# Kernel optimization log

Hardware: AMD Instinct MI355X
Metric: run time of the kernel (lower is better)

Reference implementation:

```python
import jax, jax.numpy as jnp
import numpy as np
import math

B, S, E, H = 4, 2048, 1024, 16

def setup_inputs() -> dict:
    key = jax.random.key(0)
    k1, k2, k3 = jax.random.split(key, 3)
    scale_in = 1.0 / math.sqrt(E)
    x = jax.random.normal(k1, (B, S, E), dtype=jnp.float32)
    W_attn = jax.random.normal(k2, (E, 3 * E), dtype=jnp.float32) * scale_in
    b_attn = jnp.zeros((3 * E,), dtype=jnp.float32)
    W_proj = jax.random.normal(k3, (E, E), dtype=jnp.float32) * scale_in
    b_proj = jnp.zeros((E,), dtype=jnp.float32)
    return {"x": x, "W_attn": W_attn, "b_attn": b_attn, "W_proj": W_proj, "b_proj": b_proj}

def reference(x, W_attn, b_attn, W_proj, b_proj):
    batch, seq, emb = x.shape
    hd = emb // H  # head_dim
    qkv = x @ W_attn + b_attn                      # [B,S,3E]
    q, k, v = jnp.split(qkv, 3, axis=-1)
    # [B,S,E] -> [B,H,S,hd]
    q = q.reshape(batch, seq, H, hd).transpose(0, 2, 1, 3)
    k = k.reshape(batch, seq, H, hd).transpose(0, 2, 1, 3)
    v = v.reshape(batch, seq, H, hd).transpose(0, 2, 1, 3)
    scores = jnp.einsum('bhqd,bhkd->bhqk', q, k) * (1.0 / math.sqrt(hd))
    causal = jnp.tril(jnp.ones((seq, seq), dtype=bool))
    scores = jnp.where(causal[None, None, :, :], scores, jnp.finfo(scores.dtype).min)
    attn = jax.nn.softmax(scores, axis=-1)         # dropout p=0 -> identity
    out = jnp.einsum('bhqk,bhkd->bhqd', attn, v)   # [B,H,S,hd]
    out = out.transpose(0, 2, 1, 3).reshape(batch, seq, emb)
    return out @ W_proj + b_proj
```

## Files before the change

kernel.cpp:

```cpp
#include <hip/hip_runtime.h>

typedef __bf16 bf16;
typedef __bf16 bf16x8_t __attribute__((ext_vector_type(8)));
typedef __bf16 bf16x4_t __attribute__((ext_vector_type(4)));
typedef __bf16 bf16x2_t __attribute__((ext_vector_type(2)));
typedef float f32x4_t __attribute__((ext_vector_type(4)));

#define S_ 2048
#define E_ 1024
#define HD 64
#define LOG2E 1.4426950408889634f
#define QSCALE (0.125f * LOG2E)

__device__ __forceinline__ void gl_lds16(const bf16* g, bf16* l) {
  __builtin_amdgcn_global_load_lds(
      (const __attribute__((address_space(1))) unsigned int*)g,
      (__attribute__((address_space(3))) unsigned int*)l, 16, 0, 0);
}

__global__ void cvt4(const float* __restrict__ in, bf16* __restrict__ out) {
  int i = (blockIdx.x * 256 + threadIdx.x) * 4;
  float4 v = *(const float4*)(in + i);
  bf16x4_t o = { (bf16)v.x, (bf16)v.y, (bf16)v.z, (bf16)v.w };
  *(bf16x4_t*)(out + i) = o;
}

__global__ void transpose_cvt(const float* __restrict__ in, bf16* __restrict__ out,
                              int R, int C) {
  __shared__ float tile[32][33];
  int c0 = blockIdx.x * 32, r0 = blockIdx.y * 32;
  int tx = threadIdx.x & 31, ty = threadIdx.x >> 5;
#pragma unroll
  for (int i = 0; i < 32; i += 8)
    tile[ty + i][tx] = in[(size_t)(r0 + ty + i) * C + c0 + tx];
  __syncthreads();
#pragma unroll
  for (int i = 0; i < 32; i += 8)
    out[(size_t)(c0 + ty + i) * R + r0 + tx] = (bf16)tile[tx][ty + i];
}

template <int MODE>
__global__ __launch_bounds__(256, 3)
void gemm128(const bf16* __restrict__ A, const bf16* __restrict__ Bt,
             const float* __restrict__ bias,
             bf16* __restrict__ Q, bf16* __restrict__ K, bf16* __restrict__ Vt,
             float* __restrict__ Out) {
  __shared__ __align__(16) bf16 As[128 * 64];
  __shared__ __align__(16) bf16 Bs[128 * 64];
  const int tid = threadIdx.x;
  const int wave = tid >> 6, lane = tid & 63;
  const int quad = lane >> 4, l16 = lane & 15;
  const int wm = wave >> 1, wn = wave & 1;
  const int bm = blockIdx.x, bn = blockIdx.y;

  f32x4_t acc[4][4];
#pragma unroll
  for (int i = 0; i < 4; i++)
#pragma unroll
    for (int j = 0; j < 4; j++) acc[i][j] = (f32x4_t){0.f, 0.f, 0.f, 0.f};

  for (int k0 = 0; k0 < 1024; k0 += 64) {
    __syncthreads();
#pragma unroll
    for (int it = 0; it < 4; it++) {
      int id = it * 256 + tid;
      int row = id >> 3, c = id & 7;
      int sc = (c ^ (row & 7)) * 8;
      gl_lds16(A + (size_t)(bm * 128 + row) * 1024 + k0 + sc, As + id * 8);
      gl_lds16(Bt + (size_t)(bn * 128 + row) * 1024 + k0 + sc, Bs + id * 8);
    }
    __syncthreads();
#pragma unroll
    for (int ks = 0; ks < 2; ks++) {
      bf16x8_t af[4], bfr[4];
#pragma unroll
      for (int i = 0; i < 4; i++) {
        int row = wm * 64 + i * 16 + l16;
        af[i] = *(const bf16x8_t*)&As[row * 64 + (((ks * 4 + quad) ^ (row & 7)) * 8)];
      }
#pragma unroll
      for (int j = 0; j < 4; j++) {
        int row = wn * 64 + j * 16 + l16;
        bfr[j] = *(const bf16x8_t*)&Bs[row * 64 + (((ks * 4 + quad) ^ (row & 7)) * 8)];
      }
#pragma unroll
      for (int i = 0; i < 4; i++)
#pragma unroll
        for (int j = 0; j < 4; j++)
          acc[i][j] = __builtin_amdgcn_mfma_f32_16x16x32_bf16(af[i], bfr[j], acc[i][j], 0, 0, 0);
    }
  }

  if (MODE == 0) {
#pragma unroll
    for (int j = 0; j < 4; j++) {
      int n_g = bn * 128 + wn * 64 + j * 16 + l16;
      float bv = bias[n_g];
      int which = n_g >> 10;
      int cc = n_g & 1023;
      int hh = cc >> 6, dd = cc & 63;
#pragma unroll
      for (int i = 0; i < 4; i++) {
        int m0 = bm * 128 + wm * 64 + i * 16 + quad * 4;
        int bb = m0 >> 11, ss0 = m0 & 2047;
        int bhn = bb * 16 + hh;
        if (which == 2) {
          bf16x4_t pk;
#pragma unroll
          for (int r = 0; r < 4; r++) pk[r] = (bf16)(acc[i][j][r] + bv);
          *(bf16x4_t*)&Vt[((size_t)bhn * 64 + dd) * 2048 + ss0] = pk;
        } else {
          bf16* dst = (which == 0) ? Q : K;
          float scl = (which == 0) ? QSCALE : 1.f;
#pragma unroll
          for (int r = 0; r < 4; r++)
            dst[((size_t)bhn * 2048 + ss0 + r) * 64 + dd] = (bf16)((acc[i][j][r] + bv) * scl);
        }
      }
    }
  } else {
#pragma unroll
    for (int j = 0; j < 4; j++) {
      int n_g = bn * 128 + wn * 64 + j * 16 + l16;
      float bv = bias[n_g];
#pragma unroll
      for (int i = 0; i < 4; i++) {
        int m0 = bm * 128 + wm * 64 + i * 16 + quad * 4;
#pragma unroll
        for (int r = 0; r < 4; r++)
          Out[(size_t)(m0 + r) * 1024 + n_g] = acc[i][j][r] + bv;
      }
    }
  }
}

__global__ __launch_bounds__(256, 3)
void attn_kernel(const bf16* __restrict__ Q, const bf16* __restrict__ K,
                 const bf16* __restrict__ Vt, bf16* __restrict__ O) {
  __shared__ __align__(16) bf16 Ks[128 * 64];
  __shared__ __align__(16) bf16 Vs[64 * 128];
  __shared__ __align__(16) int Ps[4][32 * 36];
  const int tid = threadIdx.x;
  const int wave = tid >> 6, lane = tid & 63;
  const int quad = lane >> 4, l16 = lane & 15;
  const int qb = 15 - blockIdx.x, bh = blockIdx.y;
  const int b = bh >> 4, h = bh & 15;

  const bf16* Qg = Q + (size_t)bh * S_ * HD;
  const bf16* Kg = K + (size_t)bh * S_ * HD;
  const bf16* Vg = Vt + (size_t)bh * HD * S_;
  int* Pw = &Ps[wave][0];

  bf16x8_t qf[2][2];
#pragma unroll
  for (int ni = 0; ni < 2; ni++)
#pragma unroll
    for (int ks = 0; ks < 2; ks++)
      qf[ni][ks] = *(const bf16x8_t*)(Qg +
          (size_t)(qb * 128 + wave * 32 + ni * 16 + l16) * HD + ks * 32 + quad * 8);

  f32x4_t o[4][2];
#pragma unroll
  for (int mi = 0; mi < 4; mi++)
#pragma unroll
    for (int ni = 0; ni < 2; ni++) o[mi][ni] = (f32x4_t){0.f, 0.f, 0.f, 0.f};
  float m_[2] = {-1e30f, -1e30f}, l_[2] = {0.f, 0.f};

  for (int kb = 0; kb <= qb; kb++) {
    __syncthreads();
    const bf16* Ksrc = Kg + (size_t)kb * 128 * HD;
#pragma unroll
    for (int it = 0; it < 4; it++) {
      int id = it * 256 + tid;
      {
        int row = id >> 3, c = id & 7;
        gl_lds16(Ksrc + row * 64 + ((c ^ (row & 7)) * 8), Ks + id * 8);
      }
      {
        int d = id >> 4, c = id & 15;
        gl_lds16(Vg + (size_t)d * S_ + kb * 128 + ((c ^ (d & 7)) * 8), Vs + id * 8);
      }
    }
    __syncthreads();

    const bool diag = (kb == qb);
#pragma unroll
    for (int hh = 0; hh < 2; hh++) {
      if (diag && hh == 1 && wave < 2) continue;

      f32x4_t sacc[4][2];
#pragma unroll
      for (int mi = 0; mi < 4; mi++)
#pragma unroll
        for (int ni = 0; ni < 2; ni++) sacc[mi][ni] = (f32x4_t){0.f, 0.f, 0.f, 0.f};
#pragma unroll
      for (int ks = 0; ks < 2; ks++)
#pragma unroll
        for (int mi = 0; mi < 4; mi++) {
          int kr = hh * 64 + mi * 16 + l16;
          bf16x8_t kf = *(const bf16x8_t*)&Ks[kr * 64 + (((ks * 4 + quad) ^ (kr & 7)) * 8)];
          sacc[mi][0] = __builtin_amdgcn_mfma_f32_16x16x32_bf16(kf, qf[0][ks], sacc[mi][0], 0, 0, 0);
          sacc[mi][1] = __builtin_amdgcn_mfma_f32_16x16x32_bf16(kf, qf[1][ks], sacc[mi][1], 0, 0, 0);
        }

      if (diag) {
#pragma unroll
        for (int mi = 0; mi < 4; mi++)
#pragma unroll
          for (int ni = 0; ni < 2; ni++) {
            int qrow = wave * 32 + ni * 16 + l16;
            int krow = hh * 64 + mi * 16 + quad * 4;
#pragma unroll
            for (int r = 0; r < 4; r++)
              if (krow + r > qrow) sacc[mi][ni][r] = -1e30f;
          }
      }

#pragma unroll
      for (int ni = 0; ni < 2; ni++) {
        float mx = -1e30f;
#pragma unroll
        for (int mi = 0; mi < 4; mi++)
#pragma unroll
          for (int r = 0; r < 4; r++) mx = fmaxf(mx, sacc[mi][ni][r]);
        mx = fmaxf(mx, __shfl_xor(mx, 16));
        mx = fmaxf(mx, __shfl_xor(mx, 32));
        float mnew = fmaxf(m_[ni], mx);
        float alpha = __builtin_amdgcn_exp2f(m_[ni] - mnew);
        m_[ni] = mnew;
        float rs = 0.f;
#pragma unroll
        for (int mi = 0; mi < 4; mi++)
#pragma unroll
          for (int r = 0; r < 4; r++) {
            float p = __builtin_amdgcn_exp2f(sacc[mi][ni][r] - mnew);
            sacc[mi][ni][r] = p;
            rs += p;
          }
        rs += __shfl_xor(rs, 16);
        rs += __shfl_xor(rs, 32);
        l_[ni] = alpha * l_[ni] + rs;
#pragma unroll
        for (int mi = 0; mi < 4; mi++)
#pragma unroll
          for (int r = 0; r < 4; r++) o[mi][ni][r] *= alpha;
      }

#pragma unroll
      for (int ni = 0; ni < 2; ni++) {
        int qr = ni * 16 + l16;
#pragma unroll
        for (int mi = 0; mi < 4; mi++) {
          bf16x2_t w0 = { (bf16)sacc[mi][ni][0], (bf16)sacc[mi][ni][1] };
          bf16x2_t w1 = { (bf16)sacc[mi][ni][2], (bf16)sacc[mi][ni][3] };
          int2 w; w.x = __builtin_bit_cast(int, w0); w.y = __builtin_bit_cast(int, w1);
          *(int2*)&Pw[qr * 36 + mi * 8 + quad * 2] = w;
        }
      }

#pragma unroll
      for (int ks2 = 0; ks2 < 2; ks2++) {
        bf16x8_t vb[4];
#pragma unroll
        for (int mi = 0; mi < 4; mi++) {
          int d = mi * 16 + l16;
          vb[mi] = *(const bf16x8_t*)&Vs[d * 128 + (((hh * 8 + ks2 * 4 + quad) ^ (d & 7)) * 8)];
        }
#pragma unroll
        for (int ni = 0; ni < 2; ni++) {
          int4 rw = *(const int4*)&Pw[(ni * 16 + l16) * 36 + ks2 * 16 + quad * 4];
          bf16x8_t pa = __builtin_bit_cast(bf16x8_t, rw);
#pragma unroll
          for (int mi = 0; mi < 4; mi++)
            o[mi][ni] = __builtin_amdgcn_mfma_f32_16x16x32_bf16(vb[mi], pa, o[mi][ni], 0, 0, 0);
        }
      }
    }
  }

#pragma unroll
  for (int ni = 0; ni < 2; ni++) {
    float inv = 1.0f / l_[ni];
    int q_g = qb * 128 + wave * 32 + ni * 16 + l16;
    size_t rowb = (size_t)(b * S_ + q_g) * E_ + h * HD;
#pragma unroll
    for (int mi = 0; mi < 4; mi++) {
      bf16x4_t ov;
#pragma unroll
      for (int r = 0; r < 4; r++) ov[r] = (bf16)(o[mi][ni][r] * inv);
      *(bf16x4_t*)&O[rowb + mi * 16 + quad * 4] = ov;
    }
  }
}

extern "C" void kernel_launch(void* const* d_in, const int* in_sizes, int n_in,
                              void* d_out, int out_size, void* d_ws, size_t ws_size,
                              hipStream_t stream) {
  const float* x      = (const float*)d_in[0];
  const float* W_attn = (const float*)d_in[1];
  const float* b_attn = (const float*)d_in[2];
  const float* W_proj = (const float*)d_in[3];
  const float* b_proj = (const float*)d_in[4];
  float* out = (float*)d_out;

  bf16* xb  = (bf16*)d_ws;
  bf16* Wat = xb + 8388608ull;
  bf16* Wpt = Wat + 3145728ull;
  bf16* Qb  = Wpt + 1048576ull;
  bf16* Kb  = Qb + 8388608ull;
  bf16* Vtb = Kb + 8388608ull;
  bf16* AOb = xb;

  cvt4<<<8192, 256, 0, stream>>>(x, xb);
  transpose_cvt<<<dim3(96, 32), 256, 0, stream>>>(W_attn, Wat, 1024, 3072);
  transpose_cvt<<<dim3(32, 32), 256, 0, stream>>>(W_proj, Wpt, 1024, 1024);
  gemm128<0><<<dim3(64, 24), 256, 0, stream>>>(xb, Wat, b_attn, Qb, Kb, Vtb, nullptr);
  attn_kernel<<<dim3(16, 64), 256, 0, stream>>>(Qb, Kb, Vtb, AOb);
  gemm128<1><<<dim3(64, 8), 256, 0, stream>>>(AOb, Wpt, b_proj, nullptr, nullptr, nullptr, out);
}
```

Before: 282.0 us.

## Rewrite attention with 32x32 MFMA, register P shuffle and paired causal tiles

The attention kernel now runs two-wave blocks in which each wave handles 64 query rows. The waves are paired so that one takes query tile t and the other takes 31-t, which balances causal work across blocks. QK and PV use 32x32x16 bf16 MFMAs, and the P matrix is repacked in registers through lane shuffles instead of being staged in LDS. The intent is to cut LDS traffic and causal load imbalance. The cost is more registers, lower occupancy per block, and a wave that idles on K/V tiles it does not need while still joining the loads and barriers.

```diff
diff --git a/kernel.cpp b/kernel.cpp
--- a/kernel.cpp
+++ b/kernel.cpp
@@ -5,6 +5,7 @@
 typedef __bf16 bf16x4_t __attribute__((ext_vector_type(4)));
 typedef __bf16 bf16x2_t __attribute__((ext_vector_type(2)));
 typedef float f32x4_t __attribute__((ext_vector_type(4)));
+typedef float f32x16_t __attribute__((ext_vector_type(16)));
 
 #define S_ 2048
 #define E_ 1024
@@ -16,6 +17,11 @@
   __builtin_amdgcn_global_load_lds(
       (const __attribute__((address_space(1))) unsigned int*)g,
       (__attribute__((address_space(3))) unsigned int*)l, 16, 0, 0);
+}
+
+__device__ __forceinline__ int pk2(float a, float b) {
+  bf16x2_t t = { (bf16)a, (bf16)b };
+  return __builtin_bit_cast(int, t);
 }
 
 __global__ void cvt4(const float* __restrict__ in, bf16* __restrict__ out) {
@@ -134,44 +140,47 @@
   }
 }
 
-__global__ __launch_bounds__(256, 3)
+__global__ __launch_bounds__(128, 2)
 void attn_kernel(const bf16* __restrict__ Q, const bf16* __restrict__ K,
                  const bf16* __restrict__ Vt, bf16* __restrict__ O) {
   __shared__ __align__(16) bf16 Ks[128 * 64];
   __shared__ __align__(16) bf16 Vs[64 * 128];
-  __shared__ __align__(16) int Ps[4][32 * 36];
   const int tid = threadIdx.x;
   const int wave = tid >> 6, lane = tid & 63;
-  const int quad = lane >> 4, l16 = lane & 15;
-  const int qb = 15 - blockIdx.x, bh = blockIdx.y;
-  const int b = bh >> 4, h = bh & 15;
+  const int c31 = lane & 31, h = lane >> 5;
+  const int blk = blockIdx.x;
+  const int bh = blk & 63, pid = blk >> 6;
+  const int b = bh >> 4, hq = bh & 15;
+  const int t = wave ? (31 - pid) : pid;
+  const int kmax = t >> 1;
+  const int kend = (31 - pid) >> 1;
+  const int q0 = t * 64;
 
   const bf16* Qg = Q + (size_t)bh * S_ * HD;
   const bf16* Kg = K + (size_t)bh * S_ * HD;
   const bf16* Vg = Vt + (size_t)bh * HD * S_;
-  int* Pw = &Ps[wave][0];
-
-  bf16x8_t qf[2][2];
+
+  bf16x8_t qf[2][4];
 #pragma unroll
   for (int ni = 0; ni < 2; ni++)
 #pragma unroll
-    for (int ks = 0; ks < 2; ks++)
+    for (int ks = 0; ks < 4; ks++)
       qf[ni][ks] = *(const bf16x8_t*)(Qg +
-          (size_t)(qb * 128 + wave * 32 + ni * 16 + l16) * HD + ks * 32 + quad * 8);
-
-  f32x4_t o[4][2];
-#pragma unroll
-  for (int mi = 0; mi < 4; mi++)
-#pragma unroll
-    for (int ni = 0; ni < 2; ni++) o[mi][ni] = (f32x4_t){0.f, 0.f, 0.f, 0.f};
+          (size_t)(q0 + ni * 32 + c31) * HD + ks * 16 + h * 8);
+
+  f32x16_t o[2][2];
+#pragma unroll
+  for (int mi = 0; mi < 2; mi++)
+#pragma unroll
+    for (int ni = 0; ni < 2; ni++) o[mi][ni] = (f32x16_t)(0.f);
   float m_[2] = {-1e30f, -1e30f}, l_[2] = {0.f, 0.f};
 
-  for (int kb = 0; kb <= qb; kb++) {
+  for (int kb = 0; kb <= kend; kb++) {
     __syncthreads();
     const bf16* Ksrc = Kg + (size_t)kb * 128 * HD;
 #pragma unroll
-    for (int it = 0; it < 4; it++) {
-      int id = it * 256 + tid;
+    for (int it = 0; it < 8; it++) {
+      int id = it * 128 + tid;
       {
         int row = id >> 3, c = id & 7;
         gl_lds16(Ksrc + row * 64 + ((c ^ (row & 7)) * 8), Ks + id * 8);
@@ -182,37 +191,44 @@
       }
     }
     __syncthreads();
-
-    const bool diag = (kb == qb);
+    if (kb > kmax) continue;
+
+    const bool diag = (kb == kmax);
 #pragma unroll
     for (int hh = 0; hh < 2; hh++) {
-      if (diag && hh == 1 && wave < 2) continue;
-
-      f32x4_t sacc[4][2];
-#pragma unroll
-      for (int mi = 0; mi < 4; mi++)
-#pragma unroll
-        for (int ni = 0; ni < 2; ni++) sacc[mi][ni] = (f32x4_t){0.f, 0.f, 0.f, 0.f};
-#pragma unroll
-      for (int ks = 0; ks < 2; ks++)
-#pragma unroll
-        for (int mi = 0; mi < 4; mi++) {
-          int kr = hh * 64 + mi * 16 + l16;
-          bf16x8_t kf = *(const bf16x8_t*)&Ks[kr * 64 + (((ks * 4 + quad) ^ (kr & 7)) * 8)];
-          sacc[mi][0] = __builtin_amdgcn_mfma_f32_16x16x32_bf16(kf, qf[0][ks], sacc[mi][0], 0, 0, 0);
-          sacc[mi][1] = __builtin_amdgcn_mfma_f32_16x16x32_bf16(kf, qf[1][ks], sacc[mi][1], 0, 0, 0);
+      if (diag && !(t & 1) && hh == 1) continue;
+
+      f32x16_t sa[2][2];
+#pragma unroll
+      for (int mi = 0; mi < 2; mi++)
+#pragma unroll
+        for (int ni = 0; ni < 2; ni++) sa[mi][ni] = (f32x16_t)(0.f);
+#pragma unroll
+      for (int ks = 0; ks < 4; ks++) {
+        bf16x8_t kf[2];
+#pragma unroll
+        for (int mi = 0; mi < 2; mi++) {
+          int krow = hh * 64 + mi * 32 + c31;
+          kf[mi] = *(const bf16x8_t*)&Ks[krow * 64 + (((ks * 2 + h) ^ (krow & 7)) * 8)];
         }
-
-      if (diag) {
-#pragma unroll
-        for (int mi = 0; mi < 4; mi++)
+#pragma unroll
+        for (int mi = 0; mi < 2; mi++)
+#pragma unroll
+          for (int ni = 0; ni < 2; ni++)
+            sa[mi][ni] = __builtin_amdgcn_mfma_f32_32x32x16_bf16(kf[mi], qf[ni][ks], sa[mi][ni], 0, 0, 0);
+      }
+
+      if (diag && (hh == 1 || !(t & 1))) {
+#pragma unroll
+        for (int mi = 0; mi < 2; mi++)
 #pragma unroll
           for (int ni = 0; ni < 2; ni++) {
-            int qrow = wave * 32 + ni * 16 + l16;
-            int krow = hh * 64 + mi * 16 + quad * 4;
-#pragma unroll
-            for (int r = 0; r < 4; r++)
-              if (krow + r > qrow) sacc[mi][ni][r] = -1e30f;
+            int ql = (t & 1) * 64 + ni * 32 + c31;
+#pragma unroll
+            for (int r = 0; r < 16; r++) {
+              int kl = hh * 64 + mi * 32 + (r & 3) + 8 * (r >> 2) + 4 * h;
+              if (kl > ql) sa[mi][ni][r] = -1e30f;
+            }
           }
       }
 
@@ -220,59 +236,63 @@
       for (int ni = 0; ni < 2; ni++) {
         float mx = -1e30f;
 #pragma unroll
-        for (int mi = 0; mi < 4; mi++)
-#pragma unroll
-          for (int r = 0; r < 4; r++) mx = fmaxf(mx, sacc[mi][ni][r]);
-        mx = fmaxf(mx, __shfl_xor(mx, 16));
+        for (int mi = 0; mi < 2; mi++)
+#pragma unroll
+          for (int r = 0; r < 16; r++) mx = fmaxf(mx, sa[mi][ni][r]);
         mx = fmaxf(mx, __shfl_xor(mx, 32));
         float mnew = fmaxf(m_[ni], mx);
         float alpha = __builtin_amdgcn_exp2f(m_[ni] - mnew);
         m_[ni] = mnew;
         float rs = 0.f;
 #pragma unroll
-        for (int mi = 0; mi < 4; mi++)
-#pragma unroll
-          for (int r = 0; r < 4; r++) {
-            float p = __builtin_amdgcn_exp2f(sacc[mi][ni][r] - mnew);
-            sacc[mi][ni][r] = p;
+        for (int mi = 0; mi < 2; mi++)
+#pragma unroll
+          for (int r = 0; r < 16; r++) {
+            float p = __builtin_amdgcn_exp2f(sa[mi][ni][r] - mnew);
+            sa[mi][ni][r] = p;
             rs += p;
           }
-        rs += __shfl_xor(rs, 16);
         rs += __shfl_xor(rs, 32);
         l_[ni] = alpha * l_[ni] + rs;
 #pragma unroll
-        for (int mi = 0; mi < 4; mi++)
-#pragma unroll
-          for (int r = 0; r < 4; r++) o[mi][ni][r] *= alpha;
-      }
-
-#pragma unroll
-      for (int ni = 0; ni < 2; ni++) {
-        int qr = ni * 16 + l16;
-#pragma unroll
-        for (int mi = 0; mi < 4; mi++) {
-          bf16x2_t w0 = { (bf16)sacc[mi][ni][0], (bf16)sacc[mi][ni][1] };
-          bf16x2_t w1 = { (bf16)sacc[mi][ni][2], (bf16)sacc[mi][ni][3] };
-          int2 w; w.x = __builtin_bit_cast(int, w0); w.y = __builtin_bit_cast(int, w1);
-          *(int2*)&Pw[qr * 36 + mi * 8 + quad * 2] = w;
-        }
-      }
-
-#pragma unroll
-      for (int ks2 = 0; ks2 < 2; ks2++) {
-        bf16x8_t vb[4];
-#pragma unroll
-        for (int mi = 0; mi < 4; mi++) {
-          int d = mi * 16 + l16;
-          vb[mi] = *(const bf16x8_t*)&Vs[d * 128 + (((hh * 8 + ks2 * 4 + quad) ^ (d & 7)) * 8)];
-        }
+        for (int mi = 0; mi < 2; mi++)
+#pragma unroll
+          for (int r = 0; r < 16; r++) o[mi][ni][r] *= alpha;
+      }
+
+#pragma unroll
+      for (int mi = 0; mi < 2; mi++) {
+        bf16x8_t va[2][2];
+#pragma unroll
+        for (int tt = 0; tt < 2; tt++)
+#pragma unroll
+          for (int mi2 = 0; mi2 < 2; mi2++) {
+            int d = mi2 * 32 + c31;
+            int cv = hh * 8 + (2 * mi + tt) * 2 + h;
+            va[tt][mi2] = *(const bf16x8_t*)&Vs[d * 128 + ((cv ^ (d & 7)) * 8)];
+          }
 #pragma unroll
         for (int ni = 0; ni < 2; ni++) {
-          int4 rw = *(const int4*)&Pw[(ni * 16 + l16) * 36 + ks2 * 16 + quad * 4];
-          bf16x8_t pa = __builtin_bit_cast(bf16x8_t, rw);
-#pragma unroll
-          for (int mi = 0; mi < 4; mi++)
-            o[mi][ni] = __builtin_amdgcn_mfma_f32_16x16x32_bf16(vb[mi], pa, o[mi][ni], 0, 0, 0);
+          int p[8], x[8];
+#pragma unroll
+          for (int w = 0; w < 8; w++) p[w] = pk2(sa[mi][ni][2 * w], sa[mi][ni][2 * w + 1]);
+#pragma unroll
+          for (int w = 0; w < 8; w++) x[w] = __shfl_xor(p[w], 32);
+          int4 w0, w1;
+          if (h == 0) {
+            w0 = make_int4(p[0], p[1], x[0], x[1]);
+            w1 = make_int4(p[4], p[5], x[4], x[5]);
+          } else {
+            w0 = make_int4(x[2], x[3], p[2], p[3]);
+            w1 = make_int4(x[6], x[7], p[6], p[7]);
+          }
+          bf16x8_t pb0 = __builtin_bit_cast(bf16x8_t, w0);
+          bf16x8_t pb1 = __builtin_bit_cast(bf16x8_t, w1);
+#pragma unroll
+          for (int mi2 = 0; mi2 < 2; mi2++) {
+            o[mi2][ni] = __builtin_amdgcn_mfma_f32_32x32x16_bf16(va[0][mi2], pb0, o[mi2][ni], 0, 0, 0);
+            o[mi2][ni] = __builtin_amdgcn_mfma_f32_32x32x16_bf16(va[1][mi2], pb1, o[mi2][ni], 0, 0, 0);
+          }
         }
       }
     }
@@ -281,15 +301,18 @@
 #pragma unroll
   for (int ni = 0; ni < 2; ni++) {
     float inv = 1.0f / l_[ni];
-    int q_g = qb * 128 + wave * 32 + ni * 16 + l16;
-    size_t rowb = (size_t)(b * S_ + q_g) * E_ + h * HD;
-#pragma unroll
-    for (int mi = 0; mi < 4; mi++) {
-      bf16x4_t ov;
-#pragma unroll
-      for (int r = 0; r < 4; r++) ov[r] = (bf16)(o[mi][ni][r] * inv);
-      *(bf16x4_t*)&O[rowb + mi * 16 + quad * 4] = ov;
-    }
+    int q_g = q0 + ni * 32 + c31;
+    size_t rowb = (size_t)(b * S_ + q_g) * E_ + hq * HD;
+#pragma unroll
+    for (int mi2 = 0; mi2 < 2; mi2++)
+#pragma unroll
+      for (int g = 0; g < 4; g++) {
+        int d0 = mi2 * 32 + 8 * g + 4 * h;
+        bf16x4_t ov;
+#pragma unroll
+        for (int r = 0; r < 4; r++) ov[r] = (bf16)(o[mi2][ni][4 * g + r] * inv);
+        *(bf16x4_t*)&O[rowb + d0] = ov;
+      }
   }
 }
 
@@ -315,6 +338,6 @@
   transpose_cvt<<<dim3(96, 32), 256, 0, stream>>>(W_attn, Wat, 1024, 3072);
   transpose_cvt<<<dim3(32, 32), 256, 0, stream>>>(W_proj, Wpt, 1024, 1024);
   gemm128<0><<<dim3(64, 24), 256, 0, stream>>>(xb, Wat, b_attn, Qb, Kb, Vtb, nullptr);
-  attn_kernel<<<dim3(16, 64), 256, 0, stream>>>(Qb, Kb, Vtb, AOb);
+  attn_kernel<<<1024, 128, 0, stream>>>(Qb, Kb, Vtb, AOb);
   gemm128<1><<<dim3(64, 8), 256, 0, stream>>>(AOb, Wpt, b_proj, nullptr, nullptr, nullptr, out);
 }
```

Result: faster. 270.5 us (-4.1%).
